# Performance work log

Hardware: AMD Instinct MI355X
Metric: run time of the kernel (lower is better)

## Reference

```python
import jax, jax.numpy as jnp
from jax import lax
import numpy as np

VOCAB, EMBED, HID, MAXLEN, BATCH = 50000, 512, 1024, 100, 512
FORGET_BIAS = 2.0


def setup_inputs() -> dict:
    key = jax.random.key(0)
    ks = jax.random.split(key, 12)
    s = 0.02
    input_queries = jax.random.randint(ks[0], (BATCH, MAXLEN), 0, VOCAB, dtype=jnp.int32)
    input_replies = jax.random.randint(ks[1], (BATCH, MAXLEN), 0, VOCAB, dtype=jnp.int32)
    query_lengths = jnp.maximum(jax.random.randint(ks[2], (BATCH,), 0, MAXLEN, dtype=jnp.int32), 1)
    reply_lengths = jnp.maximum(jax.random.randint(ks[3], (BATCH,), 0, MAXLEN, dtype=jnp.int32), 1)
    embeddings = jax.random.normal(ks[4], (VOCAB, EMBED), dtype=jnp.float32) * s
    # shared peephole LSTM weights (reuse=True in the original): kernel over [x; h], gate order i, j, f, o
    W = jax.random.normal(ks[5], (EMBED + HID, 4 * HID), dtype=jnp.float32) * s
    b = jnp.zeros((4 * HID,), dtype=jnp.float32)
    p_i = jax.random.normal(ks[6], (HID,), dtype=jnp.float32) * s
    p_f = jax.random.normal(ks[7], (HID,), dtype=jnp.float32) * s
    p_o = jax.random.normal(ks[8], (HID,), dtype=jnp.float32) * s
    M = jax.random.normal(ks[9], (HID, HID), dtype=jnp.float32) * s
    return {
        "embeddings": embeddings, "W": W, "b": b,
        "p_i": p_i, "p_f": p_f, "p_o": p_o, "M": M,
        "input_queries": input_queries, "input_replies": input_replies,
        "query_lengths": query_lengths, "reply_lengths": reply_lengths,
    }


def _lstm_encode(x_emb, lengths, W, b, p_i, p_f, p_o):
    """Peephole LSTM (TF LSTMCell, use_peepholes=True). Returns final h at sequence_length."""
    B, L, _ = x_emb.shape
    H = p_i.shape[0]

    def step(carry, xt):
        c, h = carry
        x_t, t = xt                      # x_t: [B, E]
        z = jnp.concatenate([x_t, h], axis=-1) @ W + b   # [B, 4H]
        zi, zj, zf, zo = jnp.split(z, 4, axis=-1)
        i = jax.nn.sigmoid(zi + p_i * c)
        f = jax.nn.sigmoid(zf + FORGET_BIAS + p_f * c)
        c_new = f * c + i * jnp.tanh(zj)
        o = jax.nn.sigmoid(zo + p_o * c_new)
        h_new = o * jnp.tanh(c_new)
        valid = (t < lengths)[:, None]   # hold state past sequence_length
        return (jnp.where(valid, c_new, c), jnp.where(valid, h_new, h)), None

    init = (jnp.zeros((B, H), x_emb.dtype), jnp.zeros((B, H), x_emb.dtype))
    xs = (jnp.swapaxes(x_emb, 0, 1), jnp.arange(L, dtype=jnp.int32))
    (_, h), _ = lax.scan(step, init, xs)
    return h


def reference(embeddings, W, b, p_i, p_f, p_o, M,
              input_queries, input_replies, query_lengths, reply_lengths):
    q_emb = embeddings[input_queries]    # [B, L, E]
    r_emb = embeddings[input_replies]
    q_enc = _lstm_encode(q_emb, query_lengths, W, b, p_i, p_f, p_o)   # [B, H]
    r_enc = _lstm_encode(r_emb, reply_lengths, W, b, p_i, p_f, p_o)
    q_t = q_enc @ M                                                    # bilinear transform
    distances = q_t @ r_enc.T                                          # [B, B]
    # positives = diagonal, negatives = all off-diagonal (in-batch negatives)
    labels = jnp.eye(distances.shape[0], dtype=distances.dtype)
    # sigmoid cross entropy: softplus(x) - label * x, mean over all B*B logits
    loss = jnp.mean(jax.nn.softplus(distances) - labels * distances)
    return distances, loss
```

## Files before the change

### kernel.cpp

```cpp
#include <hip/hip_runtime.h>
#include <stdint.h>

typedef unsigned short u16;
typedef __bf16 bf16x8 __attribute__((ext_vector_type(8)));
typedef float f32x4 __attribute__((ext_vector_type(4)));

#define AS1 __attribute__((address_space(1)))
#define AS3 __attribute__((address_space(3)))

__device__ __forceinline__ void ld_lds16(const void* gp, void* lp) {
  __builtin_amdgcn_global_load_lds((AS1 void*)(void*)gp, (AS3 void*)lp, 16, 0, 0);
}

__device__ __forceinline__ u16 f2bf(float f) {
  uint32_t u = __float_as_uint(f);
  u += 0x7FFFu + ((u >> 16) & 1u);
  return (u16)(u >> 16);
}

__device__ __forceinline__ float fsig(float x) { return 1.0f / (1.0f + __expf(-x)); }
__device__ __forceinline__ float ftanhf(float x) {
  float e = __expf(-2.0f * fabsf(x));
  float t = (1.0f - e) / (1.0f + e);
  return copysignf(t, x);
}

#define LSEQ 100
#define EMB 512
#define HID 1024
#define KDIM 1536

__global__ __launch_bounds__(256) void k_step(
    const u16* __restrict__ emb, const u16* __restrict__ W2T,
    const float* __restrict__ b2, const float* __restrict__ p_i,
    const float* __restrict__ p_f, const float* __restrict__ p_o,
    const int* __restrict__ tokQ, const int* __restrict__ tokR,
    const int* __restrict__ lenQ, const int* __restrict__ lenR,
    const u16* __restrict__ h_cur, u16* __restrict__ h_nxt,
    float* __restrict__ c_st, int t)
{
  __shared__ u16 sb[4 * 16384];
  const int tid = threadIdx.x;
  const int lane = tid & 63, wid = tid >> 6;
  const int wm = wid >> 1, wn = wid & 1;
  const int lane_lo = lane & 15, lane_hi = lane >> 4;
  const int g = blockIdx.x;
  const int bx = (g & 7) * 4 + ((g >> 3) & 3);
  const int by = g >> 5;

  f32x4 acc[4][4];
  const f32x4 zz = {0.f, 0.f, 0.f, 0.f};
#pragma unroll
  for (int a = 0; a < 4; ++a)
#pragma unroll
    for (int bb = 0; bb < 4; ++bb) acc[a][bb] = zz;

  int tokv[4], rowe[4], rowi[4], ldso[4], srco[4];
#pragma unroll
  for (int j = 0; j < 4; ++j) {
    const int cbase = (j * 4 + wid) * 64;
    const int ch = cbase + lane;
    const int r = ch >> 3;
    const int srcoff = ((((ch & 7) << 4) ^ ((r & 7) << 4)) >> 1);
    const int m = by * 128 + r, e = m >> 9, i = m & 511;
    tokv[j] = (e ? tokR : tokQ)[i * LSEQ + t];
    rowe[j] = e; rowi[j] = i;
    srco[j] = srcoff;
    ldso[j] = cbase * 8;
  }

  const int colbase = bx * 128 + wn * 64;
  const int h = ((colbase >> 6) << 4) + lane_lo;
  float b2v[4];
#pragma unroll
  for (int gg = 0; gg < 4; ++gg) b2v[gg] = b2[colbase + gg * 16 + lane_lo];
  const float pi = p_i[h], pf = p_f[h], po = p_o[h];
  int lenv[4][4];
  float cold[4][4];
  u16 hprev[4][4];
#pragma unroll
  for (int mi = 0; mi < 4; ++mi)
#pragma unroll
    for (int r = 0; r < 4; ++r) {
      const int m = by * 128 + wm * 64 + mi * 16 + lane_hi * 4 + r;
      const int e = m >> 9, i = m & 511;
      lenv[mi][r] = e ? lenR[i] : lenQ[i];
      const size_t ci = (size_t)(e * 512 + i) * HID + h;
      cold[mi][r] = c_st[ci];
      hprev[mi][r] = h_cur[ci];
    }
  __builtin_amdgcn_sched_barrier(0);

  const u16* pAx[4];
  const u16* pAh[4];
  const u16* pB[4];
#pragma unroll
  for (int j = 0; j < 4; ++j) {
    const int cbase = (j * 4 + wid) * 64;
    const int r = (cbase + lane) >> 3;
    pAx[j] = emb + (size_t)tokv[j] * EMB + srco[j];
    pAh[j] = h_cur + (size_t)(rowe[j] * 512 + rowi[j]) * HID - 512 + srco[j];
    pB[j]  = W2T + (size_t)(bx * 128 + r) * KDIM + srco[j];
  }

  auto stage = [&](int kt, int buf) {
    const int kb = kt * 64;
    u16* lA = sb + buf * 16384;
    u16* lB = lA + 8192;
    const bool isx = kb < EMB;
#pragma unroll
    for (int j = 0; j < 4; ++j) ld_lds16((isx ? pAx[j] : pAh[j]) + kb, lA + ldso[j]);
#pragma unroll
    for (int j = 0; j < 4; ++j) ld_lds16(pB[j] + kb, lB + ldso[j]);
  };

  auto compute = [&](int buf) {
    const u16* lA = sb + buf * 16384;
    const u16* lB = lA + 8192;
#pragma unroll
    for (int kk = 0; kk < 2; ++kk) {
      bf16x8 aF[4], bF[4];
#pragma unroll
      for (int mi = 0; mi < 4; ++mi) {
        const int rr = wm * 64 + mi * 16 + lane_lo;
        const int byo = rr * 128 + ((kk * 64 + lane_hi * 16) ^ ((rr & 7) << 4));
        aF[mi] = *(const bf16x8*)((const char*)lA + byo);
      }
#pragma unroll
      for (int ni = 0; ni < 4; ++ni) {
        const int rr = wn * 64 + ni * 16 + lane_lo;
        const int byo = rr * 128 + ((kk * 64 + lane_hi * 16) ^ ((rr & 7) << 4));
        bF[ni] = *(const bf16x8*)((const char*)lB + byo);
      }
#pragma unroll
      for (int mi = 0; mi < 4; ++mi)
#pragma unroll
        for (int ni = 0; ni < 4; ++ni)
          acc[mi][ni] = __builtin_amdgcn_mfma_f32_16x16x32_bf16(aF[mi], bF[ni], acc[mi][ni], 0, 0, 0);
    }
  };

  stage(0, 0);
  stage(1, 1);
  stage(2, 2);

  for (int kt = 0; kt < 24; ++kt) {
    if (kt <= 21)      asm volatile("s_waitcnt vmcnt(16)" ::: "memory");
    else if (kt == 22) asm volatile("s_waitcnt vmcnt(8)" ::: "memory");
    else               asm volatile("s_waitcnt vmcnt(0)" ::: "memory");
    __builtin_amdgcn_s_barrier();
    __builtin_amdgcn_sched_barrier(0);
    if (kt < 21) stage(kt + 3, (kt + 3) & 3);
    __builtin_amdgcn_s_setprio(1);
    compute(kt & 3);
    __builtin_amdgcn_s_setprio(0);
  }

#pragma unroll
  for (int mi = 0; mi < 4; ++mi) {
#pragma unroll
    for (int r = 0; r < 4; ++r) {
      const int m = by * 128 + wm * 64 + mi * 16 + lane_hi * 4 + r;
      const int e = m >> 9, i = m & 511;
      const size_t ci = (size_t)(e * 512 + i) * HID + h;
      u16 hv;
      if (t < lenv[mi][r]) {
        const float c_old = cold[mi][r];
        const float zi = acc[mi][0][r] + b2v[0] + pi * c_old;
        const float zj = acc[mi][1][r] + b2v[1];
        const float zf = acc[mi][2][r] + b2v[2] + pf * c_old;
        const float zo = acc[mi][3][r] + b2v[3];
        const float ig = fsig(zi), fg = fsig(zf);
        const float cn = fg * c_old + ig * ftanhf(zj);
        const float og = fsig(zo + po * cn);
        const float hn = og * ftanhf(cn);
        c_st[ci] = cn;
        hv = f2bf(hn);
      } else {
        hv = hprev[mi][r];
      }
      h_nxt[ci] = hv;
    }
  }
}

template <int OUT_BF16>
__global__ __launch_bounds__(256) void k_gemm(
    const u16* __restrict__ A, const u16* __restrict__ Bn,
    void* __restrict__ Cout, int K, int ldc)
{
  __shared__ u16 lA[128 * 64];
  __shared__ u16 lB[128 * 64];
  const int tid = threadIdx.x;
  const int lane = tid & 63, wid = tid >> 6;
  const int wm = wid >> 1, wn = wid & 1;
  const int lane_lo = lane & 15, lane_hi = lane >> 4;
  const int bx = blockIdx.x, by = blockIdx.y;

  f32x4 acc[4][4];
  const f32x4 zz = {0.f, 0.f, 0.f, 0.f};
#pragma unroll
  for (int a = 0; a < 4; ++a)
#pragma unroll
    for (int bb = 0; bb < 4; ++bb) acc[a][bb] = zz;

  const int nkt = K >> 6;
  for (int kt = 0; kt < nkt; ++kt) {
    const int kb = kt * 64;
#pragma unroll
    for (int j = 0; j < 4; ++j) {
      const int cbase = (j * 4 + wid) * 64;
      const int ch = cbase + lane;
      const int r = ch >> 3;
      const int srcoff = ((((ch & 7) << 4) ^ ((r & 7) << 4)) >> 1);
      ld_lds16(A + (size_t)(by * 128 + r) * K + kb + srcoff, &lA[cbase * 8]);
    }
#pragma unroll
    for (int j = 0; j < 4; ++j) {
      const int cbase = (j * 4 + wid) * 64;
      const int ch = cbase + lane;
      const int r = ch >> 3;
      const int srcoff = ((((ch & 7) << 4) ^ ((r & 7) << 4)) >> 1);
      ld_lds16(Bn + (size_t)(bx * 128 + r) * K + kb + srcoff, &lB[cbase * 8]);
    }
    __syncthreads();
#pragma unroll
    for (int kk = 0; kk < 2; ++kk) {
      bf16x8 aF[4], bF[4];
#pragma unroll
      for (int mi = 0; mi < 4; ++mi) {
        const int rr = wm * 64 + mi * 16 + lane_lo;
        const int byo = rr * 128 + ((kk * 64 + lane_hi * 16) ^ ((rr & 7) << 4));
        aF[mi] = *(const bf16x8*)((const char*)lA + byo);
      }
#pragma unroll
      for (int ni = 0; ni < 4; ++ni) {
        const int rr = wn * 64 + ni * 16 + lane_lo;
        const int byo = rr * 128 + ((kk * 64 + lane_hi * 16) ^ ((rr & 7) << 4));
        bF[ni] = *(const bf16x8*)((const char*)lB + byo);
      }
#pragma unroll
      for (int mi = 0; mi < 4; ++mi)
#pragma unroll
        for (int ni = 0; ni < 4; ++ni)
          acc[mi][ni] = __builtin_amdgcn_mfma_f32_16x16x32_bf16(aF[mi], bF[ni], acc[mi][ni], 0, 0, 0);
    }
    __syncthreads();
  }

#pragma unroll
  for (int mi = 0; mi < 4; ++mi)
#pragma unroll
    for (int r = 0; r < 4; ++r) {
      const int m = by * 128 + wm * 64 + mi * 16 + lane_hi * 4 + r;
#pragma unroll
      for (int ni = 0; ni < 4; ++ni) {
        const int col = bx * 128 + wn * 64 + ni * 16 + lane_lo;
        const float v = acc[mi][ni][r];
        if (OUT_BF16) ((u16*)Cout)[(size_t)m * ldc + col] = f2bf(v);
        else ((float*)Cout)[(size_t)m * ldc + col] = v;
      }
    }
}

__global__ void k_transpose(const float* __restrict__ in, u16* __restrict__ out,
                            int K_, int N_, int perm)
{
  __shared__ float tile[64][65];
  const int tid = threadIdx.x;
  const int k0 = blockIdx.y * 64, n0 = blockIdx.x * 64;
  const int c = tid & 63, rq = tid >> 6;
  for (int rr = 0; rr < 64; rr += 4)
    tile[rr + rq][c] = in[(size_t)(k0 + rr + rq) * N_ + n0 + c];
  __syncthreads();
  for (int nr0 = 0; nr0 < 64; nr0 += 4) {
    const int nr = nr0 + rq;
    const int n = n0 + nr;
    int np = n;
    if (perm) {
      const int g = n >> 10, hh = n & 1023;
      np = ((hh >> 4) << 6) + (g << 4) + (hh & 15);
    }
    out[(size_t)np * K_ + k0 + c] = f2bf(tile[c][nr]);
  }
}

__global__ void k_bias(const float* __restrict__ b, float* __restrict__ b2) {
  const int n = blockIdx.x * 256 + threadIdx.x;
  if (n < 4096) {
    const int g = n >> 10, hh = n & 1023;
    const int np = ((hh >> 4) << 6) + (g << 4) + (hh & 15);
    b2[np] = b[n] + (g == 2 ? 2.0f : 0.0f);
  }
}

__global__ void k_cvt(const float4* __restrict__ in, u16* __restrict__ out, size_t n4) {
  size_t idx = (size_t)blockIdx.x * blockDim.x + threadIdx.x;
  const size_t stride = (size_t)gridDim.x * blockDim.x;
  for (; idx < n4; idx += stride) {
    const float4 v = in[idx];
    ushort4 o;
    o.x = f2bf(v.x); o.y = f2bf(v.y); o.z = f2bf(v.z); o.w = f2bf(v.w);
    *(ushort4*)(out + idx * 4) = o;
  }
}

__global__ void k_zero(uint4* __restrict__ p, size_t n) {
  size_t idx = (size_t)blockIdx.x * blockDim.x + threadIdx.x;
  const size_t stride = (size_t)gridDim.x * blockDim.x;
  const uint4 z = {0u, 0u, 0u, 0u};
  for (; idx < n; idx += stride) p[idx] = z;
}

__global__ void k_loss1(const float* __restrict__ D, float* __restrict__ part) {
  __shared__ float sd[256];
  const int tid = threadIdx.x;
  float s = 0.f;
  for (int idx = blockIdx.x * 256 + tid; idx < 512 * 512; idx += 256 * 256) {
    const float x = D[idx];
    float sp;
    if (x > 20.f) sp = x;
    else if (x < -20.f) sp = __expf(x);
    else sp = __logf(1.0f + __expf(x));
    if ((idx >> 9) == (idx & 511)) sp -= x;
    s += sp;
  }
  sd[tid] = s;
  __syncthreads();
  for (int o = 128; o > 0; o >>= 1) { if (tid < o) sd[tid] += sd[tid + o]; __syncthreads(); }
  if (tid == 0) part[blockIdx.x] = sd[0];
}

__global__ void k_loss2(const float* __restrict__ part, float* __restrict__ out) {
  __shared__ float sd[256];
  const int tid = threadIdx.x;
  sd[tid] = part[tid];
  __syncthreads();
  for (int o = 128; o > 0; o >>= 1) { if (tid < o) sd[tid] += sd[tid + o]; __syncthreads(); }
  if (tid == 0) out[0] = sd[0] * (1.0f / (512.0f * 512.0f));
}

extern "C" void kernel_launch(void* const* d_in, const int* in_sizes, int n_in,
                              void* d_out, int out_size, void* d_ws, size_t ws_size,
                              hipStream_t stream)
{
  const float* embF = (const float*)d_in[0];
  const float* W    = (const float*)d_in[1];
  const float* b    = (const float*)d_in[2];
  const float* p_i  = (const float*)d_in[3];
  const float* p_f  = (const float*)d_in[4];
  const float* p_o  = (const float*)d_in[5];
  const float* Mm   = (const float*)d_in[6];
  const int* tokQ   = (const int*)d_in[7];
  const int* tokR   = (const int*)d_in[8];
  const int* lenQ   = (const int*)d_in[9];
  const int* lenR   = (const int*)d_in[10];
  float* out = (float*)d_out;

  char* ws = (char*)d_ws;
  const size_t OFF_EMB  = 0;
  const size_t OFF_W2T  = 51200000;
  const size_t OFF_MT   = OFF_W2T + 12582912;
  const size_t OFF_B2   = OFF_MT + 2097152;
  const size_t OFF_H    = OFF_B2 + 16384;
  const size_t OFF_C    = OFF_H + 4194304;
  const size_t OFF_QT   = OFF_C + 4194304;
  const size_t OFF_PART = OFF_QT + 1048576;
  const size_t NEED = OFF_PART + 1024;
  if (ws_size < NEED) return;

  u16* embB  = (u16*)(ws + OFF_EMB);
  u16* W2T   = (u16*)(ws + OFF_W2T);
  u16* MT    = (u16*)(ws + OFF_MT);
  float* b2  = (float*)(ws + OFF_B2);
  u16* hbuf  = (u16*)(ws + OFF_H);
  float* cst = (float*)(ws + OFF_C);
  u16* qt    = (u16*)(ws + OFF_QT);
  float* part= (float*)(ws + OFF_PART);

  k_cvt<<<dim3(2048), dim3(256), 0, stream>>>((const float4*)embF, embB, (size_t)(50000 * 512 / 4));
  k_transpose<<<dim3(64, 24), dim3(256), 0, stream>>>(W, W2T, 1536, 4096, 1);
  k_transpose<<<dim3(16, 16), dim3(256), 0, stream>>>(Mm, MT, 1024, 1024, 0);
  k_bias<<<dim3(16), dim3(256), 0, stream>>>(b, b2);
  k_zero<<<dim3(256), dim3(256), 0, stream>>>((uint4*)hbuf, 131072);
  k_zero<<<dim3(256), dim3(256), 0, stream>>>((uint4*)cst, 262144);

  const size_t HBUFSTRIDE = (size_t)2 * 512 * 1024;
  for (int t = 0; t < 100; ++t) {
    u16* hc = hbuf + (size_t)(t & 1) * HBUFSTRIDE;
    u16* hn = hbuf + (size_t)((t + 1) & 1) * HBUFSTRIDE;
    k_step<<<dim3(256), dim3(256), 0, stream>>>(embB, W2T, b2, p_i, p_f, p_o,
                                                tokQ, tokR, lenQ, lenR, hc, hn, cst, t);
  }

  k_gemm<1><<<dim3(8, 4), dim3(256), 0, stream>>>(hbuf, MT, qt, 1024, 1024);
  k_gemm<0><<<dim3(4, 4), dim3(256), 0, stream>>>(qt, hbuf + (size_t)512 * 1024, out, 1024, 512);

  k_loss1<<<dim3(256), dim3(256), 0, stream>>>(out, part);
  k_loss2<<<dim3(1), dim3(256), 0, stream>>>(part, out + 262144);
}
```

Before: 2.205 ms.

## Pre-pack W in MFMA fragment layout and load B straight to registers

The weight matrix is repacked at setup into a fragment-major layout, so each wave loads its B operand directly from global memory into registers with a 3-deep register pipeline, bypassing LDS. The step kernel moves to 512 threads (8 waves, 2x4 wave grid), and each wave computes 32 gate columns instead of 64. The gate layout is reorganised so each lane pair exchanges i/f and j/o values through a lane shuffle, and only half the lanes write state. LDS use is halved and per-wave B staging is removed, but the register-held B buffers add register pressure, and half the lanes do redundant gate math.

```diff
diff --git a/kernel.cpp b/kernel.cpp
--- a/kernel.cpp
+++ b/kernel.cpp
@@ -30,8 +30,8 @@
 #define HID 1024
 #define KDIM 1536
 
-__global__ __launch_bounds__(256) void k_step(
-    const u16* __restrict__ emb, const u16* __restrict__ W2T,
+__global__ __launch_bounds__(512, 2) void k_step(
+    const u16* __restrict__ emb, const u16* __restrict__ Wfm,
     const float* __restrict__ b2, const float* __restrict__ p_i,
     const float* __restrict__ p_f, const float* __restrict__ p_o,
     const int* __restrict__ tokQ, const int* __restrict__ tokR,
@@ -39,41 +39,39 @@
     const u16* __restrict__ h_cur, u16* __restrict__ h_nxt,
     float* __restrict__ c_st, int t)
 {
-  __shared__ u16 sb[4 * 16384];
+  __shared__ u16 sb[4 * 8192];
   const int tid = threadIdx.x;
   const int lane = tid & 63, wid = tid >> 6;
-  const int wm = wid >> 1, wn = wid & 1;
+  const int wm = wid >> 2, wn = wid & 3;
   const int lane_lo = lane & 15, lane_hi = lane >> 4;
   const int g = blockIdx.x;
   const int bx = (g & 7) * 4 + ((g >> 3) & 3);
   const int by = g >> 5;
 
-  f32x4 acc[4][4];
+  f32x4 acc[4][2];
   const f32x4 zz = {0.f, 0.f, 0.f, 0.f};
 #pragma unroll
   for (int a = 0; a < 4; ++a)
 #pragma unroll
-    for (int bb = 0; bb < 4; ++bb) acc[a][bb] = zz;
-
-  int tokv[4], rowe[4], rowi[4], ldso[4], srco[4];
-#pragma unroll
-  for (int j = 0; j < 4; ++j) {
-    const int cbase = (j * 4 + wid) * 64;
-    const int ch = cbase + lane;
+    for (int bb = 0; bb < 2; ++bb) acc[a][bb] = zz;
+
+  int tokv[2], rowe[2], rowi[2], ldso[2], srco[2];
+#pragma unroll
+  for (int j = 0; j < 2; ++j) {
+    const int ch = j * 512 + tid;
     const int r = ch >> 3;
-    const int srcoff = ((((ch & 7) << 4) ^ ((r & 7) << 4)) >> 1);
+    const int srcoff = ((ch & 7) ^ (r & 7)) * 8;
     const int m = by * 128 + r, e = m >> 9, i = m & 511;
     tokv[j] = (e ? tokR : tokQ)[i * LSEQ + t];
     rowe[j] = e; rowi[j] = i;
     srco[j] = srcoff;
-    ldso[j] = cbase * 8;
-  }
-
-  const int colbase = bx * 128 + wn * 64;
-  const int h = ((colbase >> 6) << 4) + lane_lo;
-  float b2v[4];
-#pragma unroll
-  for (int gg = 0; gg < 4; ++gg) b2v[gg] = b2[colbase + gg * 16 + lane_lo];
+    ldso[j] = ch * 8;
+  }
+
+  const int h = (bx * 4 + wn) * 8 + (lane & 7);
+  float b2v[2];
+#pragma unroll
+  for (int ni = 0; ni < 2; ++ni) b2v[ni] = b2[bx * 128 + wn * 32 + ni * 16 + lane_lo];
   const float pi = p_i[h], pf = p_f[h], po = p_o[h];
   int lenv[4][4];
   float cold[4][4];
@@ -91,95 +89,104 @@
     }
   __builtin_amdgcn_sched_barrier(0);
 
-  const u16* pAx[4];
-  const u16* pAh[4];
-  const u16* pB[4];
-#pragma unroll
-  for (int j = 0; j < 4; ++j) {
-    const int cbase = (j * 4 + wid) * 64;
-    const int r = (cbase + lane) >> 3;
+  const u16* pAx[2];
+  const u16* pAh[2];
+#pragma unroll
+  for (int j = 0; j < 2; ++j) {
     pAx[j] = emb + (size_t)tokv[j] * EMB + srco[j];
     pAh[j] = h_cur + (size_t)(rowe[j] * 512 + rowi[j]) * HID - 512 + srco[j];
-    pB[j]  = W2T + (size_t)(bx * 128 + r) * KDIM + srco[j];
-  }
-
-  auto stage = [&](int kt, int buf) {
+  }
+  const u16* pWl = Wfm + (size_t)(bx * 4 + wn) * 49152 + lane * 8;
+
+  bf16x8 Bst[3][4];
+
+  auto stageA = [&](int kt) {
     const int kb = kt * 64;
-    u16* lA = sb + buf * 16384;
-    u16* lB = lA + 8192;
+    u16* lA = sb + (kt & 3) * 8192;
     const bool isx = kb < EMB;
 #pragma unroll
-    for (int j = 0; j < 4; ++j) ld_lds16((isx ? pAx[j] : pAh[j]) + kb, lA + ldso[j]);
-#pragma unroll
-    for (int j = 0; j < 4; ++j) ld_lds16(pB[j] + kb, lB + ldso[j]);
+    for (int j = 0; j < 2; ++j) ld_lds16((isx ? pAx[j] : pAh[j]) + kb, lA + ldso[j]);
   };
 
-  auto compute = [&](int buf) {
-    const u16* lA = sb + buf * 16384;
-    const u16* lB = lA + 8192;
+  auto loadB = [&](int kt) {
+    const int s = kt % 3;
+#pragma unroll
+    for (int q = 0; q < 4; ++q)
+      Bst[s][q] = *(const bf16x8*)(pWl + kt * 2048 + q * 512);
+  };
+
+  auto compute = [&](int kt) {
+    const char* lA = (const char*)(sb + (kt & 3) * 8192);
+    const int s = kt % 3;
 #pragma unroll
     for (int kk = 0; kk < 2; ++kk) {
-      bf16x8 aF[4], bF[4];
+      bf16x8 aF[4];
 #pragma unroll
       for (int mi = 0; mi < 4; ++mi) {
         const int rr = wm * 64 + mi * 16 + lane_lo;
         const int byo = rr * 128 + ((kk * 64 + lane_hi * 16) ^ ((rr & 7) << 4));
-        aF[mi] = *(const bf16x8*)((const char*)lA + byo);
+        aF[mi] = *(const bf16x8*)(lA + byo);
       }
 #pragma unroll
-      for (int ni = 0; ni < 4; ++ni) {
-        const int rr = wn * 64 + ni * 16 + lane_lo;
-        const int byo = rr * 128 + ((kk * 64 + lane_hi * 16) ^ ((rr & 7) << 4));
-        bF[ni] = *(const bf16x8*)((const char*)lB + byo);
-      }
-#pragma unroll
       for (int mi = 0; mi < 4; ++mi)
 #pragma unroll
-        for (int ni = 0; ni < 4; ++ni)
-          acc[mi][ni] = __builtin_amdgcn_mfma_f32_16x16x32_bf16(aF[mi], bF[ni], acc[mi][ni], 0, 0, 0);
+        for (int ni = 0; ni < 2; ++ni)
+          acc[mi][ni] = __builtin_amdgcn_mfma_f32_16x16x32_bf16(aF[mi], Bst[s][kk * 2 + ni], acc[mi][ni], 0, 0, 0);
     }
   };
 
-  stage(0, 0);
-  stage(1, 1);
-  stage(2, 2);
-
+  stageA(0); loadB(0);
+  stageA(1); loadB(1);
+  stageA(2); loadB(2);
+
+#pragma unroll
   for (int kt = 0; kt < 24; ++kt) {
-    if (kt <= 21)      asm volatile("s_waitcnt vmcnt(16)" ::: "memory");
-    else if (kt == 22) asm volatile("s_waitcnt vmcnt(8)" ::: "memory");
+    if (kt <= 21)      asm volatile("s_waitcnt vmcnt(12)" ::: "memory");
+    else if (kt == 22) asm volatile("s_waitcnt vmcnt(6)" ::: "memory");
     else               asm volatile("s_waitcnt vmcnt(0)" ::: "memory");
     __builtin_amdgcn_s_barrier();
     __builtin_amdgcn_sched_barrier(0);
-    if (kt < 21) stage(kt + 3, (kt + 3) & 3);
+    if (kt < 21) stageA(kt + 3);
     __builtin_amdgcn_s_setprio(1);
-    compute(kt & 3);
+    compute(kt);
     __builtin_amdgcn_s_setprio(0);
-  }
-
+    __builtin_amdgcn_sched_barrier(0);
+    if (kt < 21) loadB(kt + 3);
+  }
+
+#pragma unroll
+  for (int mi = 0; mi < 4; ++mi)
+#pragma unroll
+    for (int ni = 0; ni < 2; ++ni)
+#pragma unroll
+      for (int r = 0; r < 4; ++r) acc[mi][ni][r] += b2v[ni];
+
+  const bool lo8 = (lane & 8) == 0;
 #pragma unroll
   for (int mi = 0; mi < 4; ++mi) {
 #pragma unroll
     for (int r = 0; r < 4; ++r) {
+      const float a0 = acc[mi][0][r], a1 = acc[mi][1][r];
+      const float p0 = __shfl_xor(a0, 8);
+      const float p1 = __shfl_xor(a1, 8);
+      const float zi = lo8 ? a0 : p0;
+      const float zf = lo8 ? a1 : p1;
+      const float zj = lo8 ? p0 : a0;
+      const float zo = lo8 ? p1 : a1;
       const int m = by * 128 + wm * 64 + mi * 16 + lane_hi * 4 + r;
       const int e = m >> 9, i = m & 511;
       const size_t ci = (size_t)(e * 512 + i) * HID + h;
-      u16 hv;
       if (t < lenv[mi][r]) {
         const float c_old = cold[mi][r];
-        const float zi = acc[mi][0][r] + b2v[0] + pi * c_old;
-        const float zj = acc[mi][1][r] + b2v[1];
-        const float zf = acc[mi][2][r] + b2v[2] + pf * c_old;
-        const float zo = acc[mi][3][r] + b2v[3];
-        const float ig = fsig(zi), fg = fsig(zf);
+        const float ig = fsig(zi + pi * c_old);
+        const float fg = fsig(zf + pf * c_old);
         const float cn = fg * c_old + ig * ftanhf(zj);
         const float og = fsig(zo + po * cn);
         const float hn = og * ftanhf(cn);
-        c_st[ci] = cn;
-        hv = f2bf(hn);
+        if (lo8) { c_st[ci] = cn; h_nxt[ci] = f2bf(hn); }
       } else {
-        hv = hprev[mi][r];
+        if (lo8) h_nxt[ci] = hprev[mi][r];
       }
-      h_nxt[ci] = hv;
     }
   }
 }
@@ -263,8 +270,39 @@
     }
 }
 
+__global__ void k_pack(const float* __restrict__ W, u16* __restrict__ Wfm) {
+  __shared__ float tile[64][65];
+  const int n0 = blockIdx.x * 64;
+  const int k0 = blockIdx.y * 64;
+  const int tid = threadIdx.x;
+  const int c = tid & 63, rq = tid >> 6;
+  for (int rr = 0; rr < 64; rr += 4)
+    tile[rr + rq][c] = W[(size_t)(k0 + rr + rq) * 4096 + n0 + c];
+  __syncthreads();
+  const int g = n0 >> 10;
+  const int h0 = n0 & 1023;
+  const int kt = k0 >> 6;
+  for (int cc = tid; cc < 512; cc += 256) {
+    const int hg = cc >> 6;
+    const int h7 = (cc >> 3) & 7;
+    const int k8 = cc & 7;
+    const int wq = (h0 >> 3) + hg;
+    const int gl = g * 8 + h7;
+    const int lane = (k8 & 3) * 16 + (gl & 15);
+    const int ni = gl >> 4;
+    const int kk = k8 >> 2;
+    u16 oc[8];
+#pragma unroll
+    for (int e = 0; e < 8; ++e)
+      oc[e] = f2bf(tile[k8 * 8 + e][hg * 8 + h7]);
+    const size_t o = ((((size_t)wq * 24 + kt) * 4 + kk * 2 + ni) * 64 + lane) * 8;
+    *(ushort4*)(Wfm + o)     = *(ushort4*)&oc[0];
+    *(ushort4*)(Wfm + o + 4) = *(ushort4*)&oc[4];
+  }
+}
+
 __global__ void k_transpose(const float* __restrict__ in, u16* __restrict__ out,
-                            int K_, int N_, int perm)
+                            int K_, int N_)
 {
   __shared__ float tile[64][65];
   const int tid = threadIdx.x;
@@ -275,22 +313,16 @@
   __syncthreads();
   for (int nr0 = 0; nr0 < 64; nr0 += 4) {
     const int nr = nr0 + rq;
-    const int n = n0 + nr;
-    int np = n;
-    if (perm) {
-      const int g = n >> 10, hh = n & 1023;
-      np = ((hh >> 4) << 6) + (g << 4) + (hh & 15);
-    }
-    out[(size_t)np * K_ + k0 + c] = f2bf(tile[c][nr]);
+    out[(size_t)(n0 + nr) * K_ + k0 + c] = f2bf(tile[c][nr]);
   }
 }
 
 __global__ void k_bias(const float* __restrict__ b, float* __restrict__ b2) {
-  const int n = blockIdx.x * 256 + threadIdx.x;
-  if (n < 4096) {
-    const int g = n >> 10, hh = n & 1023;
-    const int np = ((hh >> 4) << 6) + (g << 4) + (hh & 15);
-    b2[np] = b[n] + (g == 2 ? 2.0f : 0.0f);
+  const int np = blockIdx.x * 256 + threadIdx.x;
+  if (np < 4096) {
+    const int g = (np >> 3) & 3;
+    const int h = (np >> 5) * 8 + (np & 7);
+    b2[np] = b[g * 1024 + h] + (g == 2 ? 2.0f : 0.0f);
   }
 }
 
@@ -359,8 +391,8 @@
 
   char* ws = (char*)d_ws;
   const size_t OFF_EMB  = 0;
-  const size_t OFF_W2T  = 51200000;
-  const size_t OFF_MT   = OFF_W2T + 12582912;
+  const size_t OFF_WFM  = 51200000;
+  const size_t OFF_MT   = OFF_WFM + 12582912;
   const size_t OFF_B2   = OFF_MT + 2097152;
   const size_t OFF_H    = OFF_B2 + 16384;
   const size_t OFF_C    = OFF_H + 4194304;
@@ -370,7 +402,7 @@
   if (ws_size < NEED) return;
 
   u16* embB  = (u16*)(ws + OFF_EMB);
-  u16* W2T   = (u16*)(ws + OFF_W2T);
+  u16* Wfm   = (u16*)(ws + OFF_WFM);
   u16* MT    = (u16*)(ws + OFF_MT);
   float* b2  = (float*)(ws + OFF_B2);
   u16* hbuf  = (u16*)(ws + OFF_H);
@@ -379,8 +411,8 @@
   float* part= (float*)(ws + OFF_PART);
 
   k_cvt<<<dim3(2048), dim3(256), 0, stream>>>((const float4*)embF, embB, (size_t)(50000 * 512 / 4));
-  k_transpose<<<dim3(64, 24), dim3(256), 0, stream>>>(W, W2T, 1536, 4096, 1);
-  k_transpose<<<dim3(16, 16), dim3(256), 0, stream>>>(Mm, MT, 1024, 1024, 0);
+  k_pack<<<dim3(64, 24), dim3(256), 0, stream>>>(W, Wfm);
+  k_transpose<<<dim3(16, 16), dim3(256), 0, stream>>>(Mm, MT, 1024, 1024);
   k_bias<<<dim3(16), dim3(256), 0, stream>>>(b, b2);
   k_zero<<<dim3(256), dim3(256), 0, stream>>>((uint4*)hbuf, 131072);
   k_zero<<<dim3(256), dim3(256), 0, stream>>>((uint4*)cst, 262144);
@@ -389,7 +421,7 @@
   for (int t = 0; t < 100; ++t) {
     u16* hc = hbuf + (size_t)(t & 1) * HBUFSTRIDE;
     u16* hn = hbuf + (size_t)((t + 1) & 1) * HBUFSTRIDE;
-    k_step<<<dim3(256), dim3(256), 0, stream>>>(embB, W2T, b2, p_i, p_f, p_o,
+    k_step<<<dim3(256), dim3(512), 0, stream>>>(embB, Wfm, b2, p_i, p_f, p_o,
                                                 tokQ, tokR, lenQ, lenR, hc, hn, cst, t);
   }
 
```

After: 2.357 ms. 6.9% more time.
